# Kernel tuning notes

Measured on AMD Instinct MI355X. Metric: run time of the kernel, lower is better.

## Reference

```python
import jax, jax.numpy as jnp
import numpy as np
import math

# Module configuration (matches init_kwargs)
BATCH = 4
C_IN = 16
C_OUT = 16
GROUPS = 16
NR = 3                      # isotropic kernel_shape -> kernel_size = 3 hat basis fns
H_IN = W_IN = 1024
H_OUT = W_OUT = 512
SCALE_H = H_IN // H_OUT     # conv stride
SCALE_W = W_IN // W_OUT
DOMAIN = (2.0, 2.0)
R_CUTOFF = max(DOMAIN[0] / H_OUT, DOMAIN[1] / W_OUT)          # default radius_cutoff
PSI_H = math.floor(2 * R_CUTOFF * H_IN / DOMAIN[0]) + 1       # = 5
PSI_W = math.floor(2 * R_CUTOFF * W_IN / DOMAIN[1]) + 1       # = 5
Q_WEIGHT = DOMAIN[0] * DOMAIN[1] / (H_IN * W_IN)              # quadrature weight dA
EPS = 1e-9


def _build_psi() -> np.ndarray:
    """Precompute the local DISCO filter basis psi: (NR, PSI_H, PSI_W).

    Isotropic 'hat' basis functions of the radial distance, evaluated on the
    local equidistant window around the origin, then discretely normalized by
    the quadrature weights (transpose_normalization=False, single output pt).
    """
    ys = np.linspace(-R_CUTOFF, R_CUTOFF, PSI_H)
    xs = np.linspace(-R_CUTOFF, R_CUTOFF, PSI_W)
    yy, xx = np.meshgrid(ys, xs, indexing="ij")
    r = np.sqrt(xx ** 2 + yy ** 2)                              # (PSI_H, PSI_W)
    dr = R_CUTOFF / NR
    k = np.arange(NR, dtype=np.float64)[:, None, None]
    vals = np.maximum(0.0, 1.0 - np.abs(r[None] - k * dr) / dr)
    vals = vals * (r[None] <= R_CUTOFF)
    # normalization: each basis fn integrates to 1 under the quadrature rule
    norm = vals.sum(axis=(1, 2), keepdims=True) * Q_WEIGHT + EPS
    return (vals / norm).astype(np.float32)


def setup_inputs() -> dict:
    key = jax.random.key(0)
    k1, k2 = jax.random.split(key)
    x = jax.random.normal(k1, (BATCH, C_IN, H_IN, W_IN), dtype=jnp.float32)
    groupsize = C_IN // GROUPS                                  # = 1
    scale = math.sqrt(1.0 / groupsize)
    weight = scale * jax.random.normal(k2, (C_OUT, groupsize, NR), dtype=jnp.float32)
    bias = jnp.zeros((C_OUT,), dtype=jnp.float32)
    psi = jnp.asarray(_build_psi())
    return {"x": x, "weight": weight, "bias": bias, "psi": psi}


def reference(x, weight, bias, psi):
    # Assemble the effective conv kernel from learned basis coefficients:
    # weight: (C_OUT, groupsize, NR), psi: (NR, PSI_H, PSI_W)
    kernel = Q_WEIGHT * jnp.einsum("ogk,khw->oghw", weight, psi)
    ph, pw = (PSI_H - 1) // 2, (PSI_W - 1) // 2
    xp = jnp.pad(x, ((0, 0), (0, 0), (ph, ph), (pw, pw)))       # zero padding (non-periodic)
    out = jax.lax.conv_general_dilated(
        xp, kernel,
        window_strides=(SCALE_H, SCALE_W),
        padding="VALID",
        dimension_numbers=("NCHW", "OIHW", "NCHW"),
        feature_group_count=GROUPS,
    )                                                            # (B, C_OUT, H_OUT, W_OUT)
    return out + bias[None, :, None, None]
```

## Files before the change

kernel.cpp:

```cpp
#include <hip/hip_runtime.h>
#include <stdint.h>


#define H_IN   1024
#define W_IN   1024
#define H_OUT  512
#define W_OUT  512
#define CCH    16
#define BATCH  4
#define NRB    3
#define PSIW   5
#define ROWS_OUT 4
#define ROWS_IN  (2 * ROWS_OUT + 3)
#define PITCH    1032
#define QW 3.814697265625e-06f

__global__ __launch_bounds__(256) void disco_conv_kernel(
    const float* __restrict__ x,
    const float* __restrict__ weight,
    const float* __restrict__ bias,
    const float* __restrict__ psi,
    float* __restrict__ out)
{
    __shared__ __align__(16) float tile[ROWS_IN * PITCH];
    __shared__ float kbuf[32];

    const int t  = threadIdx.x;
    const int i0 = blockIdx.x * ROWS_OUT;
    const int o  = blockIdx.y;
    const int b  = blockIdx.z;

    const float* plane = x + (size_t)(b * CCH + o) * (H_IN * W_IN);

    if (t < 25) {
        const int dy = t / 5, dx = t % 5;
        const float w0 = weight[o * NRB + 0];
        const float w1 = weight[o * NRB + 1];
        const float w2 = weight[o * NRB + 2];
        kbuf[t] = QW * (w0 * psi[(0 * PSIW + dy) * PSIW + dx] +
                        w1 * psi[(1 * PSIW + dy) * PSIW + dx] +
                        w2 * psi[(2 * PSIW + dy) * PSIW + dx]);
    }

    const int y_base = 2 * i0 - 2;
    #pragma unroll
    for (int rr = 0; rr < ROWS_IN; ++rr) {
        const int y = y_base + rr;
        float4 v = make_float4(0.f, 0.f, 0.f, 0.f);
        if ((unsigned)y < (unsigned)H_IN) {
            v = *(const float4*)(plane + (size_t)y * W_IN + 4 * t);
        }
        *(float4*)&tile[rr * PITCH + 4 + 4 * t] = v;
        if (t == 0) {
            tile[rr * PITCH + 2] = 0.f;
            tile[rr * PITCH + 3] = 0.f;
        }
        if (t == 1) {
            *(float4*)&tile[rr * PITCH + 1028] = make_float4(0.f, 0.f, 0.f, 0.f);
        }
    }
    __syncthreads();

    float K[25];
    #pragma unroll
    for (int n = 0; n < 25; ++n) K[n] = kbuf[n];

    const float bo = bias[o];
    float acc[ROWS_OUT][2];
    #pragma unroll
    for (int ip = 0; ip < ROWS_OUT; ++ip) { acc[ip][0] = bo; acc[ip][1] = bo; }

    #pragma unroll
    for (int rr = 0; rr < ROWS_IN; ++rr) {
        const float* row = &tile[rr * PITCH + 4 * t];
        const float4 va = *(const float4*)(row);
        const float4 vb = *(const float4*)(row + 4);
        const float2 vc = *(const float2*)(row + 8);
        const float f[10] = { va.x, va.y, va.z, va.w,
                              vb.x, vb.y, vb.z, vb.w,
                              vc.x, vc.y };
        #pragma unroll
        for (int ip = 0; ip < ROWS_OUT; ++ip) {
            const int dy = rr - 2 * ip;
            if (dy >= 0 && dy < 5) {
                #pragma unroll
                for (int dx = 0; dx < 5; ++dx) {
                    const float kv = K[dy * 5 + dx];
                    acc[ip][0] += kv * f[2 + dx];
                    acc[ip][1] += kv * f[4 + dx];
                }
            }
        }
    }

    float* oplane = out + (size_t)(b * CCH + o) * (H_OUT * W_OUT);
    #pragma unroll
    for (int ip = 0; ip < ROWS_OUT; ++ip) {
        *(float2*)(oplane + (size_t)(i0 + ip) * W_OUT + 2 * t) =
            make_float2(acc[ip][0], acc[ip][1]);
    }
}

extern "C" void kernel_launch(void* const* d_in, const int* in_sizes, int n_in,
                              void* d_out, int out_size, void* d_ws, size_t ws_size,
                              hipStream_t stream) {
    const float* x      = (const float*)d_in[0];
    const float* weight = (const float*)d_in[1];
    const float* bias   = (const float*)d_in[2];
    const float* psi    = (const float*)d_in[3];
    float* out          = (float*)d_out;

    dim3 grid(H_OUT / ROWS_OUT, CCH, BATCH);
    disco_conv_kernel<<<grid, 256, 0, stream>>>(x, weight, bias, psi, out);
}
```

Before: 400.3 us.

## Split tiles by column halves, halve LDS footprint, use nontemporal output stores

Each block now covers half the output width (256 columns) over 4 rows, which halves the shared-memory tile. That should allow more resident blocks per CU and doubles the grid. Each thread now computes 2 rows x 2 columns instead of 4 rows x 2 columns. Output writes switch to nontemporal stores so they do not pollute the cache. In exchange, halo columns are re-read across the column split, and the tile load uses a more irregular chunked loop with per-chunk bounds checks.

```diff
diff --git a/kernel.cpp b/kernel.cpp
--- a/kernel.cpp
+++ b/kernel.cpp
@@ -7,13 +7,17 @@
 #define H_OUT  512
 #define W_OUT  512
 #define CCH    16
-#define BATCH  4
 #define NRB    3
 #define PSIW   5
 #define ROWS_OUT 4
-#define ROWS_IN  (2 * ROWS_OUT + 3)
-#define PITCH    1032
+#define ROWS_IN  11
+#define COLS_OUT 256
+#define LROW     520
+#define CHUNKS_PER_ROW (LROW / 4)
+#define NCHUNK   (ROWS_IN * CHUNKS_PER_ROW)
 #define QW 3.814697265625e-06f
+
+typedef float vf2 __attribute__((ext_vector_type(2)));
 
 __global__ __launch_bounds__(256) void disco_conv_kernel(
     const float* __restrict__ x,
@@ -22,13 +26,20 @@
     const float* __restrict__ psi,
     float* __restrict__ out)
 {
-    __shared__ __align__(16) float tile[ROWS_IN * PITCH];
+    __shared__ __align__(16) float tile[ROWS_IN * LROW];
     __shared__ float kbuf[32];
 
     const int t  = threadIdx.x;
-    const int i0 = blockIdx.x * ROWS_OUT;
+    const int bx = blockIdx.x;
+    const int ct = bx & 1;
+    const int rt = bx >> 1;
     const int o  = blockIdx.y;
     const int b  = blockIdx.z;
+
+    const int i0 = rt * ROWS_OUT;
+    const int j0 = ct * COLS_OUT;
+    const int x0 = 2 * j0 - 4;
+    const int y0 = 2 * i0 - 2;
 
     const float* plane = x + (size_t)(b * CCH + o) * (H_IN * W_IN);
 
@@ -42,21 +53,19 @@
                         w2 * psi[(2 * PSIW + dy) * PSIW + dx]);
     }
 
-    const int y_base = 2 * i0 - 2;
     #pragma unroll
-    for (int rr = 0; rr < ROWS_IN; ++rr) {
-        const int y = y_base + rr;
-        float4 v = make_float4(0.f, 0.f, 0.f, 0.f);
-        if ((unsigned)y < (unsigned)H_IN) {
-            v = *(const float4*)(plane + (size_t)y * W_IN + 4 * t);
-        }
-        *(float4*)&tile[rr * PITCH + 4 + 4 * t] = v;
-        if (t == 0) {
-            tile[rr * PITCH + 2] = 0.f;
-            tile[rr * PITCH + 3] = 0.f;
-        }
-        if (t == 1) {
-            *(float4*)&tile[rr * PITCH + 1028] = make_float4(0.f, 0.f, 0.f, 0.f);
+    for (int it = 0; it < 6; ++it) {
+        const int q = t + it * 256;
+        if (q < NCHUNK) {
+            const int rr = q / CHUNKS_PER_ROW;
+            const int m  = q - rr * CHUNKS_PER_ROW;
+            const int y  = y0 + rr;
+            const int xc = x0 + 4 * m;
+            float4 v = make_float4(0.f, 0.f, 0.f, 0.f);
+            if ((unsigned)y < (unsigned)H_IN && (unsigned)xc <= (unsigned)(W_IN - 4)) {
+                v = *(const float4*)(plane + (size_t)y * W_IN + xc);
+            }
+            *(float4*)&tile[rr * LROW + 4 * m] = v;
         }
     }
     __syncthreads();
@@ -65,40 +74,46 @@
     #pragma unroll
     for (int n = 0; n < 25; ++n) K[n] = kbuf[n];
 
+    const int c   = t & 127;
+    const int rho = t >> 7;
     const float bo = bias[o];
-    float acc[ROWS_OUT][2];
+    float a00 = bo, a01 = bo;
+    float a10 = bo, a11 = bo;
+
+    const float* base = &tile[(4 * rho) * LROW + 4 * c];
     #pragma unroll
-    for (int ip = 0; ip < ROWS_OUT; ++ip) { acc[ip][0] = bo; acc[ip][1] = bo; }
-
-    #pragma unroll
-    for (int rr = 0; rr < ROWS_IN; ++rr) {
-        const float* row = &tile[rr * PITCH + 4 * t];
+    for (int rl = 0; rl < 7; ++rl) {
+        const float* row = base + rl * LROW;
         const float4 va = *(const float4*)(row);
         const float4 vb = *(const float4*)(row + 4);
         const float2 vc = *(const float2*)(row + 8);
         const float f[10] = { va.x, va.y, va.z, va.w,
                               vb.x, vb.y, vb.z, vb.w,
                               vc.x, vc.y };
-        #pragma unroll
-        for (int ip = 0; ip < ROWS_OUT; ++ip) {
-            const int dy = rr - 2 * ip;
-            if (dy >= 0 && dy < 5) {
-                #pragma unroll
-                for (int dx = 0; dx < 5; ++dx) {
-                    const float kv = K[dy * 5 + dx];
-                    acc[ip][0] += kv * f[2 + dx];
-                    acc[ip][1] += kv * f[4 + dx];
-                }
+        if (rl < 5) {
+            #pragma unroll
+            for (int dx = 0; dx < 5; ++dx) {
+                const float kv = K[rl * 5 + dx];
+                a00 += kv * f[2 + dx];
+                a01 += kv * f[4 + dx];
+            }
+        }
+        if (rl >= 2) {
+            #pragma unroll
+            for (int dx = 0; dx < 5; ++dx) {
+                const float kv = K[(rl - 2) * 5 + dx];
+                a10 += kv * f[2 + dx];
+                a11 += kv * f[4 + dx];
             }
         }
     }
 
     float* oplane = out + (size_t)(b * CCH + o) * (H_OUT * W_OUT);
-    #pragma unroll
-    for (int ip = 0; ip < ROWS_OUT; ++ip) {
-        *(float2*)(oplane + (size_t)(i0 + ip) * W_OUT + 2 * t) =
-            make_float2(acc[ip][0], acc[ip][1]);
-    }
+    const size_t o0 = (size_t)(i0 + 2 * rho) * W_OUT + j0 + 2 * c;
+    vf2 s0; s0.x = a00; s0.y = a01;
+    vf2 s1; s1.x = a10; s1.y = a11;
+    __builtin_nontemporal_store(s0, (vf2*)(oplane + o0));
+    __builtin_nontemporal_store(s1, (vf2*)(oplane + o0 + W_OUT));
 }
 
 extern "C" void kernel_launch(void* const* d_in, const int* in_sizes, int n_in,
@@ -110,6 +125,6 @@
     const float* psi    = (const float*)d_in[3];
     float* out          = (float*)d_out;
 
-    dim3 grid(H_OUT / ROWS_OUT, CCH, BATCH);
+    dim3 grid(2 * (H_OUT / ROWS_OUT), CCH, 4);
     disco_conv_kernel<<<grid, 256, 0, stream>>>(x, weight, bias, psi, out);
 }
```

After: 381.4 us. 1.05x faster.
